# Optimization experiments

Hardware: AMD Instinct MI355X
Metric: run time of the kernel (lower is better)

The kernel has to match this reference:

```python
import jax, jax.numpy as jnp
import numpy as np

H = 1024            # hinges
S = 4               # shims
N = H + 2           # nodes
NC = 2 * N          # flattened DOFs
B = 256             # batch of independent chains
L = 1.0             # rest edge length
DT = 0.001          # integration step
GAMMA = 2.0         # damping
N_STEPS = 64        # relaxation steps (truncated scan)


def setup_inputs() -> dict:
    key = jax.random.key(0)
    k1, k2, k3, k4, k5 = jax.random.split(key, 5)
    xs = jnp.arange(N, dtype=jnp.float32) * L
    base = jnp.stack([xs, jnp.zeros(N, jnp.float32)], axis=-1)          # (N,2) straight chain
    noise = 0.01 * jax.random.normal(k1, (B, N, 2), jnp.float32)
    noise = noise.at[:, :2, :].set(0.0)                                  # nodes 0,1 fixed exactly
    pos0 = base[None] + noise                                            # (B,N,2)
    tip_base = base[-1]
    tip_off = jnp.stack([-0.1 * L * H * jax.random.uniform(k2, (B,)),
                         2.0 * jax.random.normal(k3, (B,))], axis=-1)
    tip_pos = (tip_base[None] + tip_off).astype(jnp.float32)             # (B,2) imposed tip
    thetas_ss = 0.3 * jax.random.uniform(k4, (H,), jnp.float32)          # snap-through angles
    buckle_arr = jax.random.randint(k5, (H, S), 0, 2).astype(jnp.int32)  # {0,1} -> maps to {-1,+1}
    return dict(pos0=pos0, tip_pos=tip_pos, thetas_ss=thetas_ss, buckle_arr=buckle_arr,
                k_stiff=jnp.float32(10.0), k_soft=jnp.float32(0.5), k_stretch=jnp.float32(1000.0))


def _free_mask():
    m = np.ones(NC, bool)
    m[:4] = False            # nodes 0,1 fixed (dof_idx = 2*node+comp)
    m[2 * (N - 1):] = False  # tip node imposed
    return jnp.asarray(m)


def _energy(x, thetas_ss, buckle_pm, k_stiff, k_soft, k_stretch):
    """Total potential energy of one chain; x is flattened (NC,)."""
    pos = x.reshape(N, 2)
    v1 = pos[1:-1] - pos[:-2]                 # (H,2) edge into hinge h
    v2 = pos[2:] - pos[1:-1]                  # (H,2) edge out of hinge h
    theta = jnp.arctan2(v1[:, 0] * v2[:, 1] - v1[:, 1] * v2[:, 0],
                        jnp.sum(v1 * v2, -1))               # (H,) CCW hinge angle
    d = pos[1:] - pos[:-1]
    elen = jnp.sqrt(jnp.sum(d * d, -1))                     # (H+1,) edge lengths
    T = theta[:, None]                                      # (H,1)
    TH = thetas_ss[:, None]                                 # (H,1)
    stiff = ((buckle_pm == 1) & (T < TH)) | ((buckle_pm == -1) & (T > -TH))  # (H,S)
    k_rot = jnp.where(stiff, k_stiff, k_soft)
    e_rot = 0.5 * jnp.sum(k_rot * (T - TH) ** 2)
    e_str = 0.5 * jnp.sum(k_stretch * (elen - L) ** 2)
    return e_rot + e_str


def reference(pos0, tip_pos, thetas_ss, buckle_arr, k_stiff, k_soft, k_stretch):
    buckle_pm = 2 * buckle_arr - 1                           # {0,1} -> {-1,+1}
    free = _free_mask()                                      # (NC,) static
    x0 = pos0.reshape(B, NC)
    x0 = x0.at[:, 2 * (N - 1)].set(tip_pos[:, 0]).at[:, 2 * (N - 1) + 1].set(tip_pos[:, 1])
    v0 = jnp.zeros_like(x0)

    grad_e = jax.vmap(jax.grad(
        lambda x: _energy(x, thetas_ss, buckle_pm, k_stiff, k_soft, k_stretch)))

    def step(carry, _):
        x, v = carry
        f = -grad_e(x)                                       # potential force, (B,NC)
        v = jnp.where(free[None], v + DT * (f - GAMMA * v), 0.0)
        x = jnp.where(free[None], x + DT * v, x)             # fixed/imposed DOFs held
        return (x, v), None

    (xf, _vf), _ = jax.lax.scan(step, (x0, v0), None, length=N_STEPS)
    return xf                                                # (B,NC) relaxed positions
```

## Files before the change

### kernel.cpp

```cpp
#include <hip/hip_runtime.h>

#define NN 1026
#define NA 1024
#define BLK 1024
typedef float v2f __attribute__((ext_vector_type(2)));

__device__ __forceinline__ v2f vbc(float s) { return (v2f){s, s}; }

__device__ __forceinline__ float fast_atan2f(float y, float x) {
    float ax = __builtin_fabsf(x), ay = __builtin_fabsf(y);
    float mx = fmaxf(ax, ay), mn = fminf(ax, ay);
    float a  = mn * __builtin_amdgcn_rcpf(mx);
    float s  = a * a;
    float r  = fmaf(s, -0.0117212f,  0.05265332f);
    r = fmaf(s, r, -0.11643287f);
    r = fmaf(s, r,  0.19354346f);
    r = fmaf(s, r, -0.33262347f);
    r = fmaf(s, r,  0.99997726f);
    r *= a;
    if (ay > ax)  r = 1.57079637f - r;
    if (x < 0.0f) r = 3.14159274f - r;
    return copysignf(r, y);
}

__global__ __launch_bounds__(BLK)
void equil_kernel(const float* __restrict__ pos0,
                  const float* __restrict__ tip_pos,
                  const float* __restrict__ thetas_ss,
                  const int*   __restrict__ buckle,
                  const float* __restrict__ kstiff_p,
                  const float* __restrict__ ksoft_p,
                  const float* __restrict__ kstretch_p,
                  float* __restrict__ out)
{
    __shared__ v2f    pos[NN];
    __shared__ float4 PB4[NA + 1];

    const int b = blockIdx.x;
    const int t = threadIdx.x;
    const float k_str  = kstretch_p[0];
    const float k_sd   = kstiff_p[0] - ksoft_p[0];
    const float k4soft = 4.0f * ksoft_p[0];

    const v2f* p0g = (const v2f*)(pos0 + (size_t)b * 2052);
    v2f myp;
    if (t < 1023) myp = p0g[t + 2];
    else          myp = (v2f){tip_pos[2*b], tip_pos[2*b+1]};
    pos[t + 2] = myp;
    if (t < 2) pos[t] = p0g[t];

    const float TH = thetas_ss[t];
    const int4 bk  = ((const int4*)buckle)[t];
    const float npl = (float)(bk.x + bk.y + bk.z + bk.w);
    v2f vel = vbc(0.f);
    __syncthreads();

#pragma unroll 2
    for (int s = 0; s < 64; ++s) {
        v2f pa = pos[t], pb = pos[t + 1];
        v2f v1 = pb - pa;
        v2f v2 = myp - pb;
        float l2a = fmaf(v1.x, v1.x, v1.y * v1.y);
        float l2b = fmaf(v2.x, v2.x, v2.y * v2.y);
        float cr  = v1.x * v2.y - v1.y * v2.x;
        float dt_ = fmaf(v1.x, v2.x, v1.y * v2.y);
        float theta = fast_atan2f(cr, dt_);
        float cnt = (theta <  TH ? npl        : 0.f)
                  + (theta > -TH ? 4.f - npl  : 0.f);
        float K = fmaf(cnt, k_sd, k4soft);
        float m = K * (theta - TH);
        float ila = __builtin_amdgcn_rsqf(l2a);
        float ilb = __builtin_amdgcn_rsqf(l2b);
        float m1 = m * ila * ila;
        float m2 = m * ilb * ilb;
        v2f rot1 = (v2f){ v1.y, -v1.x};
        v2f rot2 = (v2f){ v2.y, -v2.x};
        v2f Bv = vbc(-m2) * rot2;
        float sca = k_str * (1.0f - ila);
        v2f P  = vbc(sca) * v1 + vbc(m1) * rot1;
        PB4[t] = make_float4(P.x, P.y, Bv.x, Bv.y);
        if (t == NA - 1) {
            float scb = k_str * (1.0f - ilb);
            PB4[NA] = make_float4(scb * v2.x, scb * v2.y, 0.f, 0.f);
        }
        __syncthreads();

        if (t < 1023) {
            float4 n1 = PB4[t + 1];
            v2f P2 = ((const v2f*)PB4)[2 * (t + 2)];
            v2f Qm = (v2f){n1.x - n1.z, n1.y - n1.w};
            v2f f  = (P2 - Qm) - Bv;
            vel = vel + vbc(0.001f) * (f - vbc(2.0f) * vel);
            myp = myp + vbc(0.001f) * vel;
            pos[t + 2] = myp;
        }
        __syncthreads();
    }

    v2f* o = (v2f*)(out + (size_t)b * 2052);
    o[t + 2] = myp;
    if (t < 2) o[t] = pos[t];
}

extern "C" void kernel_launch(void* const* d_in, const int* in_sizes, int n_in,
                              void* d_out, int out_size, void* d_ws, size_t ws_size,
                              hipStream_t stream) {
    const float* pos0   = (const float*)d_in[0];
    const float* tip    = (const float*)d_in[1];
    const float* thetas = (const float*)d_in[2];
    const int*   buckle = (const int*)  d_in[3];
    const float* ks     = (const float*)d_in[4];
    const float* ko     = (const float*)d_in[5];
    const float* kr     = (const float*)d_in[6];
    float* out = (float*)d_out;
    hipLaunchKernelGGL(equil_kernel, dim3(256), dim3(BLK), 0, stream,
                       pos0, tip, thetas, buckle, ks, ko, kr, out);
}
```

Before: 49.98 us.

## Replace block-wide barriers with neighbor-wave LDS flag synchronization

The two __syncthreads per relaxation step are replaced by per-wave progress flags in shared memory. Each wave waits only on its left neighbor's position update and its right neighbor's force partials, so waves can drift relative to each other. This is meant to remove the full-block barrier stall across 16 waves. In exchange it adds spin-polling with s_sleep, a bounded-iteration escape, and manual lgkmcnt waits, and the shared buffer is split into separate P and Q arrays.

```diff
diff --git a/kernel.cpp b/kernel.cpp
--- a/kernel.cpp
+++ b/kernel.cpp
@@ -23,6 +23,15 @@
     return copysignf(r, y);
 }
 
+__device__ __forceinline__ void waitFlag(volatile int* f, int target) {
+    int iters = 0;
+    while (*f < target) {
+        __builtin_amdgcn_s_sleep(1);
+        if (++iters > (1 << 22)) break;
+    }
+    __asm__ __volatile__("" ::: "memory");
+}
+
 __global__ __launch_bounds__(BLK)
 void equil_kernel(const float* __restrict__ pos0,
                   const float* __restrict__ tip_pos,
@@ -33,11 +42,15 @@
                   const float* __restrict__ kstretch_p,
                   float* __restrict__ out)
 {
-    __shared__ v2f    pos[NN];
-    __shared__ float4 PB4[NA + 1];
+    __shared__ v2f pos[NN];
+    __shared__ v2f Ps[NA + 1];
+    __shared__ v2f Qs[NA];
+    __shared__ int aFlag[17];
+    __shared__ int pFlag[16];
 
     const int b = blockIdx.x;
     const int t = threadIdx.x;
+    const int w = t >> 6, l = t & 63;
     const float k_str  = kstretch_p[0];
     const float k_sd   = kstiff_p[0] - ksoft_p[0];
     const float k4soft = 4.0f * ksoft_p[0];
@@ -48,6 +61,8 @@
     else          myp = (v2f){tip_pos[2*b], tip_pos[2*b+1]};
     pos[t + 2] = myp;
     if (t < 2) pos[t] = p0g[t];
+    if (t < 17) aFlag[t] = (t == 16) ? 1000 : 0;
+    if (t < 16) pFlag[t] = 0;
 
     const float TH = thetas_ss[t];
     const int4 bk  = ((const int4*)buckle)[t];
@@ -55,8 +70,9 @@
     v2f vel = vbc(0.f);
     __syncthreads();
 
-#pragma unroll 2
-    for (int s = 0; s < 64; ++s) {
+    for (int s = 1; s <= 64; ++s) {
+        if (w > 0) waitFlag(&pFlag[w - 1], s - 1);
+
         v2f pa = pos[t], pb = pos[t + 1];
         v2f v1 = pb - pa;
         v2f v2 = myp - pb;
@@ -78,23 +94,28 @@
         v2f Bv = vbc(-m2) * rot2;
         float sca = k_str * (1.0f - ila);
         v2f P  = vbc(sca) * v1 + vbc(m1) * rot1;
-        PB4[t] = make_float4(P.x, P.y, Bv.x, Bv.y);
+        v2f Q  = P - Bv;
+        Ps[t] = P;
+        Qs[t] = Q;
         if (t == NA - 1) {
             float scb = k_str * (1.0f - ilb);
-            PB4[NA] = make_float4(scb * v2.x, scb * v2.y, 0.f, 0.f);
+            Ps[NA] = vbc(scb) * v2;
         }
-        __syncthreads();
+        __asm__ __volatile__("s_waitcnt lgkmcnt(0)" ::: "memory");
+        if (l == 0) *(volatile int*)&aFlag[w] = s;
+
+        waitFlag(&aFlag[w + 1], s);
 
         if (t < 1023) {
-            float4 n1 = PB4[t + 1];
-            v2f P2 = ((const v2f*)PB4)[2 * (t + 2)];
-            v2f Qm = (v2f){n1.x - n1.z, n1.y - n1.w};
-            v2f f  = (P2 - Qm) - Bv;
+            v2f Pn = Ps[t + 2];
+            v2f Qm = Qs[t + 1];
+            v2f f  = (Pn - Qm) - Bv;
             vel = vel + vbc(0.001f) * (f - vbc(2.0f) * vel);
             myp = myp + vbc(0.001f) * vel;
             pos[t + 2] = myp;
         }
-        __syncthreads();
+        __asm__ __volatile__("s_waitcnt lgkmcnt(0)" ::: "memory");
+        if (l == 0) *(volatile int*)&pFlag[w] = s;
     }
 
     v2f* o = (v2f*)(out + (size_t)b * 2052);
```

Result: slower. 58.08 us (+16.2%).

## Assign four nodes per thread with halo recompute and double-buffered positions

Applied to the files above, without the earlier changes.

Each block now runs 256 threads, and each thread owns four consecutive nodes. It recomputes the hinge and edge terms for its local window plus a halo of neighbouring nodes, which removes the intermediate shared force buffer. Positions live in a double-buffered shared array, so each step needs one barrier instead of two. The cost is redundant edge and angle work at the window edges (about 6 atan2 per 4 nodes) and higher register use per thread.

```diff
diff --git a/kernel.cpp b/kernel.cpp
--- a/kernel.cpp
+++ b/kernel.cpp
@@ -1,8 +1,6 @@
 #include <hip/hip_runtime.h>
 
-#define NN 1026
-#define NA 1024
-#define BLK 1024
+#define BLK 256
 typedef float v2f __attribute__((ext_vector_type(2)));
 
 __device__ __forceinline__ v2f vbc(float s) { return (v2f){s, s}; }
@@ -33,73 +31,113 @@
                   const float* __restrict__ kstretch_p,
                   float* __restrict__ out)
 {
-    __shared__ v2f    pos[NN];
-    __shared__ float4 PB4[NA + 1];
+    __shared__ v2f buf[2][1028];
 
-    const int b = blockIdx.x;
-    const int t = threadIdx.x;
+    const int b  = blockIdx.x;
+    const int t  = threadIdx.x;
+    const int n0 = 2 + 4 * t;
     const float k_str  = kstretch_p[0];
     const float k_sd   = kstiff_p[0] - ksoft_p[0];
     const float k4soft = 4.0f * ksoft_p[0];
 
     const v2f* p0g = (const v2f*)(pos0 + (size_t)b * 2052);
-    v2f myp;
-    if (t < 1023) myp = p0g[t + 2];
-    else          myp = (v2f){tip_pos[2*b], tip_pos[2*b+1]};
-    pos[t + 2] = myp;
-    if (t < 2) pos[t] = p0g[t];
+    v2f xx[4];
+    #pragma unroll
+    for (int k = 0; k < 4; ++k) xx[k] = p0g[n0 + k];
+    if (t == BLK - 1) xx[3] = (v2f){tip_pos[2*b], tip_pos[2*b+1]};
 
-    const float TH = thetas_ss[t];
-    const int4 bk  = ((const int4*)buckle)[t];
-    const float npl = (float)(bk.x + bk.y + bk.z + bk.w);
-    v2f vel = vbc(0.f);
+    #pragma unroll
+    for (int k = 0; k < 4; ++k) { buf[0][n0 + k] = xx[k]; buf[1][n0 + k] = xx[k]; }
+    if (t == 0) {
+        v2f c0 = p0g[0], c1 = p0g[1];
+        buf[0][0] = c0;  buf[1][0] = c0;
+        buf[0][1] = c1;  buf[1][1] = c1;
+        buf[0][1026] = (v2f){1.f, 0.f};  buf[1][1026] = (v2f){1.f, 0.f};
+        buf[0][1027] = (v2f){2.f, 0.f};  buf[1][1027] = (v2f){2.f, 0.f};
+    }
+
+    float TH[6], NPL[6], MSK[6];
+    #pragma unroll
+    for (int q = 0; q < 6; ++q) {
+        int j  = 4 * t + q;
+        int jc = j < 1023 ? j : 1023;
+        TH[q]  = thetas_ss[jc];
+        int4 bb = ((const int4*)buckle)[jc];
+        NPL[q] = (float)(bb.x + bb.y + bb.z + bb.w);
+        MSK[q] = (j < 1024) ? 1.f : 0.f;
+    }
+    float UM[4];
+    #pragma unroll
+    for (int k = 0; k < 4; ++k) UM[k] = (n0 + k <= 1024) ? 1.f : 0.f;
+
+    v2f vv[4];
+    #pragma unroll
+    for (int k = 0; k < 4; ++k) vv[k] = vbc(0.f);
+
     __syncthreads();
 
-#pragma unroll 2
+    int cur = 0;
     for (int s = 0; s < 64; ++s) {
-        v2f pa = pos[t], pb = pos[t + 1];
-        v2f v1 = pb - pa;
-        v2f v2 = myp - pb;
-        float l2a = fmaf(v1.x, v1.x, v1.y * v1.y);
-        float l2b = fmaf(v2.x, v2.x, v2.y * v2.y);
-        float cr  = v1.x * v2.y - v1.y * v2.x;
-        float dt_ = fmaf(v1.x, v2.x, v1.y * v2.y);
-        float theta = fast_atan2f(cr, dt_);
-        float cnt = (theta <  TH ? npl        : 0.f)
-                  + (theta > -TH ? 4.f - npl  : 0.f);
-        float K = fmaf(cnt, k_sd, k4soft);
-        float m = K * (theta - TH);
-        float ila = __builtin_amdgcn_rsqf(l2a);
-        float ilb = __builtin_amdgcn_rsqf(l2b);
-        float m1 = m * ila * ila;
-        float m2 = m * ilb * ilb;
-        v2f rot1 = (v2f){ v1.y, -v1.x};
-        v2f rot2 = (v2f){ v2.y, -v2.x};
-        v2f Bv = vbc(-m2) * rot2;
-        float sca = k_str * (1.0f - ila);
-        v2f P  = vbc(sca) * v1 + vbc(m1) * rot1;
-        PB4[t] = make_float4(P.x, P.y, Bv.x, Bv.y);
-        if (t == NA - 1) {
-            float scb = k_str * (1.0f - ilb);
-            PB4[NA] = make_float4(scb * v2.x, scb * v2.y, 0.f, 0.f);
+        const v2f* bc = buf[cur];
+        v2f X[8];
+        X[0] = bc[n0 - 2];  X[1] = bc[n0 - 1];
+        X[2] = xx[0]; X[3] = xx[1]; X[4] = xx[2]; X[5] = xx[3];
+        X[6] = bc[n0 + 4];  X[7] = bc[n0 + 5];
+
+        v2f e[7]; float il[7], il2[7];
+        #pragma unroll
+        for (int i = 0; i < 7; ++i) {
+            e[i] = X[i + 1] - X[i];
+            float l2 = fmaf(e[i].x, e[i].x, e[i].y * e[i].y);
+            il[i]  = __builtin_amdgcn_rsqf(l2);
+            il2[i] = il[i] * il[i];
         }
+
+        float mm[6];
+        #pragma unroll
+        for (int q = 0; q < 6; ++q) {
+            float cr  = e[q].x * e[q+1].y - e[q].y * e[q+1].x;
+            float dt_ = fmaf(e[q].x, e[q+1].x, e[q].y * e[q+1].y);
+            float th  = fast_atan2f(cr, dt_);
+            float cnt = (th <  TH[q] ? NPL[q]       : 0.f)
+                      + (th > -TH[q] ? 4.f - NPL[q] : 0.f);
+            float K = fmaf(cnt, k_sd, k4soft);
+            mm[q] = MSK[q] * (K * (th - TH[q]));
+        }
+
+        v2f Pp[6], Bb[5], Qq[5];
+        #pragma unroll
+        for (int q = 1; q < 6; ++q) {
+            float sc = k_str * (1.0f - il[q]);
+            float m1 = mm[q] * il2[q];
+            Pp[q] = vbc(sc) * e[q] + vbc(m1) * (v2f){e[q].y, -e[q].x};
+        }
+        #pragma unroll
+        for (int q = 0; q < 5; ++q) {
+            float m2 = mm[q] * il2[q + 1];
+            Bb[q] = (v2f){ -m2 * e[q+1].y, m2 * e[q+1].x };
+        }
+        #pragma unroll
+        for (int q = 1; q < 5; ++q) Qq[q] = Pp[q] - Bb[q];
+
+        #pragma unroll
+        for (int k = 0; k < 4; ++k) {
+            v2f f = (Pp[k+2] - Qq[k+1] - Bb[k]) * vbc(UM[k]);
+            vv[k] = vv[k] + vbc(0.001f) * (f - vbc(2.0f) * vv[k]);
+            xx[k] = xx[k] + vbc(0.001f) * vv[k];
+        }
+
+        v2f* bn = buf[cur ^ 1];
+        #pragma unroll
+        for (int k = 0; k < 4; ++k) bn[n0 + k] = xx[k];
         __syncthreads();
-
-        if (t < 1023) {
-            float4 n1 = PB4[t + 1];
-            v2f P2 = ((const v2f*)PB4)[2 * (t + 2)];
-            v2f Qm = (v2f){n1.x - n1.z, n1.y - n1.w};
-            v2f f  = (P2 - Qm) - Bv;
-            vel = vel + vbc(0.001f) * (f - vbc(2.0f) * vel);
-            myp = myp + vbc(0.001f) * vel;
-            pos[t + 2] = myp;
-        }
-        __syncthreads();
+        cur ^= 1;
     }
 
     v2f* o = (v2f*)(out + (size_t)b * 2052);
-    o[t + 2] = myp;
-    if (t < 2) o[t] = pos[t];
+    #pragma unroll
+    for (int k = 0; k < 4; ++k) o[n0 + k] = xx[k];
+    if (t == 0) { o[0] = buf[0][0]; o[1] = buf[0][1]; }
 }
 
 extern "C" void kernel_launch(void* const* d_in, const int* in_sizes, int n_in,
```

Measured after the change: 54.20 us. 1.08x slower.

## Double-buffer positions and recompute wave-boundary hinges to drop a barrier per step

Applied to the files above, without the earlier changes.

Positions are double-buffered so each step needs only one __syncthreads instead of two. Per-wavefront scratch arrays hold the force partials, and the last two lanes of each 64-lane wave recompute the neighbouring wave's hinge terms, so force assembly stays inside the wave without a block-wide barrier. The trade is extra redundant atan2/rsqrt work on two lanes per wave, some branch divergence, and dummy padding entries that keep the tip hinge finite. Correctness relies on lockstep execution within a wavefront between the shared-memory write and read.

```diff
diff --git a/kernel.cpp b/kernel.cpp
--- a/kernel.cpp
+++ b/kernel.cpp
@@ -1,7 +1,5 @@
 #include <hip/hip_runtime.h>
 
-#define NN 1026
-#define NA 1024
 #define BLK 1024
 typedef float v2f __attribute__((ext_vector_type(2)));
 
@@ -23,6 +21,27 @@
     return copysignf(r, y);
 }
 
+__device__ __forceinline__ void angle_pipe(v2f v1, v2f v2, float TH, float npl,
+                                           float msk, float k_sd, float k4soft,
+                                           float k_str, v2f& P, v2f& B) {
+    float l2a = fmaf(v1.x, v1.x, v1.y * v1.y);
+    float l2b = fmaf(v2.x, v2.x, v2.y * v2.y);
+    float cr  = v1.x * v2.y - v1.y * v2.x;
+    float dt_ = fmaf(v1.x, v2.x, v1.y * v2.y);
+    float theta = fast_atan2f(cr, dt_);
+    float cnt = (theta <  TH ? npl        : 0.f)
+              + (theta > -TH ? 4.f - npl  : 0.f);
+    float K = fmaf(cnt, k_sd, k4soft);
+    float m = msk * (K * (theta - TH));
+    float ila = __builtin_amdgcn_rsqf(l2a);
+    float ilb = __builtin_amdgcn_rsqf(l2b);
+    float m1 = m * ila * ila;
+    float m2 = m * ilb * ilb;
+    float sca = k_str * (1.0f - ila);
+    P = vbc(sca) * v1 + vbc(m1) * (v2f){v1.y, -v1.x};
+    B = vbc(-m2) * (v2f){v2.y, -v2.x};
+}
+
 __global__ __launch_bounds__(BLK)
 void equil_kernel(const float* __restrict__ pos0,
                   const float* __restrict__ tip_pos,
@@ -33,11 +52,13 @@
                   const float* __restrict__ kstretch_p,
                   float* __restrict__ out)
 {
-    __shared__ v2f    pos[NN];
-    __shared__ float4 PB4[NA + 1];
+    __shared__ v2f buf0[1028], buf1[1028];
+    __shared__ v2f PQ[16][136];
 
     const int b = blockIdx.x;
     const int t = threadIdx.x;
+    const int l = t & 63;
+    v2f* PQw = PQ[t >> 6];
     const float k_str  = kstretch_p[0];
     const float k_sd   = kstiff_p[0] - ksoft_p[0];
     const float k4soft = 4.0f * ksoft_p[0];
@@ -46,60 +67,57 @@
     v2f myp;
     if (t < 1023) myp = p0g[t + 2];
     else          myp = (v2f){tip_pos[2*b], tip_pos[2*b+1]};
-    pos[t + 2] = myp;
-    if (t < 2) pos[t] = p0g[t];
+    buf0[t + 2] = myp;  buf1[t + 2] = myp;
+    if (t < 2)  { buf0[t] = p0g[t]; buf1[t] = p0g[t]; }
+    if (t == 2) {
+        buf0[1026] = (v2f){1.f, 0.5f};   buf1[1026] = (v2f){1.f, 0.5f};
+        buf0[1027] = (v2f){2.f, 0.25f};  buf1[1027] = (v2f){2.f, 0.25f};
+    }
 
     const float TH = thetas_ss[t];
     const int4 bk  = ((const int4*)buckle)[t];
     const float npl = (float)(bk.x + bk.y + bk.z + bk.w);
+    const int   t2c  = (t + 2 < 1024) ? t + 2 : 1023;
+    const float TH2  = thetas_ss[t2c];
+    const int4  bk2  = ((const int4*)buckle)[t2c];
+    const float npl2 = (float)(bk2.x + bk2.y + bk2.z + bk2.w);
+    const float msk2 = (t + 2 < 1024) ? 1.f : 0.f;
+
     v2f vel = vbc(0.f);
     __syncthreads();
 
-#pragma unroll 2
+    v2f* br = buf0;
+    v2f* bw = buf1;
     for (int s = 0; s < 64; ++s) {
-        v2f pa = pos[t], pb = pos[t + 1];
-        v2f v1 = pb - pa;
-        v2f v2 = myp - pb;
-        float l2a = fmaf(v1.x, v1.x, v1.y * v1.y);
-        float l2b = fmaf(v2.x, v2.x, v2.y * v2.y);
-        float cr  = v1.x * v2.y - v1.y * v2.x;
-        float dt_ = fmaf(v1.x, v2.x, v1.y * v2.y);
-        float theta = fast_atan2f(cr, dt_);
-        float cnt = (theta <  TH ? npl        : 0.f)
-                  + (theta > -TH ? 4.f - npl  : 0.f);
-        float K = fmaf(cnt, k_sd, k4soft);
-        float m = K * (theta - TH);
-        float ila = __builtin_amdgcn_rsqf(l2a);
-        float ilb = __builtin_amdgcn_rsqf(l2b);
-        float m1 = m * ila * ila;
-        float m2 = m * ilb * ilb;
-        v2f rot1 = (v2f){ v1.y, -v1.x};
-        v2f rot2 = (v2f){ v2.y, -v2.x};
-        v2f Bv = vbc(-m2) * rot2;
-        float sca = k_str * (1.0f - ila);
-        v2f P  = vbc(sca) * v1 + vbc(m1) * rot1;
-        PB4[t] = make_float4(P.x, P.y, Bv.x, Bv.y);
-        if (t == NA - 1) {
-            float scb = k_str * (1.0f - ilb);
-            PB4[NA] = make_float4(scb * v2.x, scb * v2.y, 0.f, 0.f);
+        v2f pa = br[t], pb = br[t + 1];
+        v2f P, Bv;
+        angle_pipe(pb - pa, myp - pb, TH, npl, 1.f, k_sd, k4soft, k_str, P, Bv);
+        PQw[l]      = P;
+        PQw[68 + l] = P - Bv;
+
+        if (l >= 62) {
+            v2f hb = br[t + 3], hc = br[t + 4];
+            v2f Ph, Bh;
+            angle_pipe(hb - myp, hc - hb, TH2, npl2, msk2, k_sd, k4soft, k_str, Ph, Bh);
+            PQw[l + 2]      = Ph;
+            PQw[68 + l + 2] = Ph - Bh;
         }
-        __syncthreads();
 
+        v2f Pn = PQw[l + 2];
+        v2f Qm = PQw[68 + l + 1];
         if (t < 1023) {
-            float4 n1 = PB4[t + 1];
-            v2f P2 = ((const v2f*)PB4)[2 * (t + 2)];
-            v2f Qm = (v2f){n1.x - n1.z, n1.y - n1.w};
-            v2f f  = (P2 - Qm) - Bv;
+            v2f f = (Pn - Qm) - Bv;
             vel = vel + vbc(0.001f) * (f - vbc(2.0f) * vel);
             myp = myp + vbc(0.001f) * vel;
-            pos[t + 2] = myp;
         }
+        bw[t + 2] = myp;
         __syncthreads();
+        v2f* tmp = br; br = bw; bw = tmp;
     }
 
     v2f* o = (v2f*)(out + (size_t)b * 2052);
     o[t + 2] = myp;
-    if (t < 2) o[t] = pos[t];
+    if (t < 2) o[t] = buf0[t];
 }
 
 extern "C" void kernel_launch(void* const* d_in, const int* in_sizes, int n_in,
```

Result: slower. 73.21 us (+46.5%).
